# Optimization experiments

Measured on AMD Instinct MI355X. Metric: run time of the kernel, lower is better.

Reference implementation:

```python
import jax, jax.numpy as jnp
import numpy as np
from jax import lax

N = 16384
K = 16
EPS = 1e-5


def setup_inputs() -> dict:
    key = jax.random.key(0)
    ks = jax.random.split(key, 10)

    def w(k, shape):
        fan_in = shape[0]
        return jax.random.normal(k, shape, jnp.float32) / np.sqrt(fan_in)

    return {
        "pos": jax.random.normal(ks[0], (N, 3), jnp.float32),
        "normal": jax.random.normal(ks[1], (N, 3), jnp.float32),
        # conv1 mlp: Linear(9,64) -> GroupNorm(8,64) -> ReLU -> Linear(64,64)
        "W1a": w(ks[2], (9, 64)), "b1a": jnp.zeros((64,), jnp.float32),
        "g1": jnp.ones((64,), jnp.float32), "beta1": jnp.zeros((64,), jnp.float32),
        "W1b": w(ks[3], (64, 64)), "b1b": jnp.zeros((64,), jnp.float32),
        # conv2 mlp: Linear(67,64) -> GroupNorm(8,64) -> ReLU -> Linear(64,64)
        "W2a": w(ks[4], (67, 64)), "b2a": jnp.zeros((64,), jnp.float32),
        "g2": jnp.ones((64,), jnp.float32), "beta2": jnp.zeros((64,), jnp.float32),
        "W2b": w(ks[5], (64, 64)), "b2b": jnp.zeros((64,), jnp.float32),
        # conv3 mlp: Linear(67,128) -> GroupNorm(16,128) -> ReLU -> Linear(128,128)
        "W3a": w(ks[6], (67, 128)), "b3a": jnp.zeros((128,), jnp.float32),
        "g3": jnp.ones((128,), jnp.float32), "beta3": jnp.zeros((128,), jnp.float32),
        "W3b": w(ks[7], (128, 128)), "b3b": jnp.zeros((128,), jnp.float32),
    }


def knn_graph(pos, k):
    # [N,N] squared distances; loop=True -> self is included (distance 0).
    sq = jnp.sum(pos * pos, axis=1)
    d2 = sq[:, None] + sq[None, :] - 2.0 * (pos @ pos.T)
    _, nbr = lax.top_k(-d2, k)  # [N,k] neighbor (source) indices per target node
    return nbr


def group_norm(h, gamma, beta, groups):
    # h: [N,k,C]; normalize each group of channels per edge sample.
    n, k, c = h.shape
    hg = h.reshape(n, k, groups, c // groups)
    mu = hg.mean(axis=-1, keepdims=True)
    var = hg.var(axis=-1, keepdims=True)
    hg = (hg - mu) * lax.rsqrt(var + EPS)
    return hg.reshape(n, k, c) * gamma + beta


def pointnet_conv(x, pos, nbr, Wa, ba, gamma, beta, Wb, bb, groups):
    # message: concat(x_j, pos_j - pos_i), MLP per edge, max-aggregate over neighbors
    xj = x[nbr]                              # [N,k,C_in]
    rel = pos[nbr] - pos[:, None, :]         # [N,k,3]
    m = jnp.concatenate([xj, rel], axis=-1)  # [N,k,C_in+3]
    h = m @ Wa + ba
    h = jax.nn.relu(group_norm(h, gamma, beta, groups))
    h = h @ Wb + bb
    return jnp.max(h, axis=1)                # [N,C_out]


def reference(pos, normal, W1a, b1a, g1, beta1, W1b, b1b,
              W2a, b2a, g2, beta2, W2b, b2b,
              W3a, b3a, g3, beta3, W3b, b3b):
    nbr = knn_graph(pos, K)
    h = jnp.concatenate([pos, normal], axis=-1)  # [N,6]
    h1 = jax.nn.relu(pointnet_conv(h, pos, nbr, W1a, b1a, g1, beta1, W1b, b1b, 8))
    h2 = jax.nn.relu(pointnet_conv(h1, pos, nbr, W2a, b2a, g2, beta2, W2b, b2b, 8))
    h3 = jax.nn.relu(pointnet_conv(h2, pos, nbr, W3a, b3a, g3, beta3, W3b, b3b, 16))
    return (h1, h2, h3)
```

## Files before the change

kernel.cpp:

```cpp
#include <hip/hip_runtime.h>
#include <hip/hip_bf16.h>
#include <stdint.h>

typedef unsigned long long u64;
typedef unsigned int u32;
typedef __attribute__((ext_vector_type(8))) short bf16x8;
typedef __attribute__((ext_vector_type(8))) unsigned short u16x8;
typedef __attribute__((ext_vector_type(4))) float f32x4;

__device__ __forceinline__ float ldv(const void* p, size_t idx, int mode) {
  return mode ? __bfloat162float(((const __hip_bfloat16*)p)[idx])
              : ((const float*)p)[idx];
}
__device__ __forceinline__ void stv(void* p, size_t idx, int mode, float v) {
  if (mode) ((__hip_bfloat16*)p)[idx] = __float2bfloat16(v);
  else      ((float*)p)[idx] = v;
}
__device__ __forceinline__ unsigned short f2bfb(float f) {
  u32 u = __float_as_uint(f);
  u32 r = u + 0x7fffu + ((u >> 16) & 1u);
  return (unsigned short)(r >> 16);
}
__device__ __forceinline__ float bfb2f(unsigned short b) {
  return __uint_as_float((u32)b << 16);
}
__device__ __forceinline__ u64 shfl64(u64 v, int src) {
  int lo = __shfl((int)(u32)(v & 0xffffffffu), src, 64);
  int hi = __shfl((int)(u32)(v >> 32), src, 64);
  return ((u64)(u32)hi << 32) | (u32)lo;
}
__device__ __forceinline__ u64 shflxor64(u64 v, int m) {
  int lo = __shfl_xor((int)(u32)(v & 0xffffffffu), m, 64);
  int hi = __shfl_xor((int)(u32)(v >> 32), m, 64);
  return ((u64)(u32)hi << 32) | (u32)lo;
}
__device__ __forceinline__ u64 shfl64w16(u64 v, int src) {
  int lo = __shfl((int)(u32)(v & 0xffffffffu), src, 16);
  int hi = __shfl((int)(u32)(v >> 32), src, 16);
  return ((u64)(u32)hi << 32) | (u32)lo;
}

__global__ void PointNetSimple_61409442398998_kernel() {}

struct CvtEnt { const void* src; float* dst; int n; };
struct CvtArgs { CvtEnt e[12]; };
struct WEnt { const void* src; unsigned short* dst; int K, N, Kpad; };
struct WArgs { WEnt e[6]; };

__global__ void setup_kernel(const void* __restrict__ pos,
                             const void* __restrict__ nrm,
                             WArgs wa, CvtArgs ca,
                             int* __restrict__ flag,
                             float4* __restrict__ pos4,
                             float* __restrict__ h0, int n) {
  const unsigned short* u16p = (const unsigned short*)pos;
  int cnt = 0;
  for (int k = 0; k < 32; ++k) {
    int e = (u16p[k] >> 7) & 0xff;
    if (e >= 110 && e <= 140) cnt++;
  }
  const int mode = (cnt >= 26) ? 1 : 0;

  const int nprep = n >> 8;
  const int b = blockIdx.x;
  if (b < nprep) {
    int i = b * 256 + threadIdx.x;
    float x = ldv(pos, 3*(size_t)i+0, mode);
    float y = ldv(pos, 3*(size_t)i+1, mode);
    float z = ldv(pos, 3*(size_t)i+2, mode);
    pos4[i] = make_float4(x, y, z, x*x + y*y + z*z);
    h0[6*(size_t)i+0] = x; h0[6*(size_t)i+1] = y; h0[6*(size_t)i+2] = z;
    h0[6*(size_t)i+3] = ldv(nrm, 3*(size_t)i+0, mode);
    h0[6*(size_t)i+4] = ldv(nrm, 3*(size_t)i+1, mode);
    h0[6*(size_t)i+5] = ldv(nrm, 3*(size_t)i+2, mode);
  } else {
    int r = b - nprep;
    if (r < 6) {
      WEnt ent = wa.e[r];
      for (int t = threadIdx.x; t < ent.N * ent.Kpad; t += blockDim.x) {
        int nn = t / ent.Kpad;
        int k  = t - nn * ent.Kpad;
        float v = (k < ent.K) ? ldv(ent.src, (size_t)k * ent.N + nn, mode) : 0.0f;
        ent.dst[t] = f2bfb(v);
      }
      if (r == 0 && threadIdx.x == 0) flag[0] = mode;
    } else {
      for (int t2 = 0; t2 < 12; ++t2) {
        CvtEnt ent = ca.e[t2];
        for (int t = threadIdx.x; t < ent.n; t += blockDim.x)
          ent.dst[t] = ldv(ent.src, t, mode);
      }
    }
  }
}

#define KNN_TPB 512
#define KNN_WPB 8
#define KCH 1024

__device__ __forceinline__ void knn_flush(u64* __restrict__ wbuf, int& cnt,
                                          u64& val, u64& t15, float& th,
                                          int lane) {
  u64 cand = (lane < cnt) ? wbuf[lane] : ~0ull;
#pragma unroll
  for (int k = 2; k <= 64; k <<= 1) {
#pragma unroll
    for (int j = k >> 1; j > 0; j >>= 1) {
      u64 other = shflxor64(cand, j);
      bool up    = ((lane & k) == 0) || (k == 64);
      bool lower = ((lane & j) == 0);
      bool keepMin = (up == lower);
      u64 mn = cand < other ? cand : other;
      u64 mx = cand < other ? other : cand;
      cand = keepMin ? mn : mx;
    }
  }
  u64 rev = shfl64w16(cand, 15 - (lane & 15));
  u64 lo = val < rev ? val : rev;
#pragma unroll
  for (int j = 8; j > 0; j >>= 1) {
    u64 other = shflxor64(lo, j);
    bool lower = ((lane & j) == 0);
    u64 mn = lo < other ? lo : other;
    u64 mx = lo < other ? other : lo;
    lo = lower ? mn : mx;
  }
  val = (lane < 16) ? lo : ~0ull;
  t15 = shfl64(val, 15);
  th = __uint_as_float((u32)(t15 >> 32));
  cnt = 0;
}

__global__ __launch_bounds__(KNN_TPB) void knn4_kernel(
    const float4* __restrict__ pos4, int* __restrict__ nbr, int n) {
  __shared__ float4 sp[2][KCH];
  __shared__ u64 buf[KNN_WPB][72];
  const int tid  = threadIdx.x;
  const int lane = tid & 63;
  const int wid  = tid >> 6;
  const int i    = blockIdx.x * KNN_WPB + wid;
  const float4 pi = pos4[i];
  u64* wbuf = &buf[wid][0];

  u64 val = ~0ull;
  u64 t15 = ~0ull;
  float th = 3.4e38f;
  int cnt = 0;

  for (int t = tid; t < KCH; t += KNN_TPB) sp[0][t] = pos4[t];
  __syncthreads();

  const int nch = n / KCH;
  for (int c = 0; c < nch; ++c) {
    const int cur = c & 1;
    float4 pre0, pre1;
    const bool more = (c + 1 < nch);
    if (more) {
      pre0 = pos4[(size_t)(c+1)*KCH + tid];
      pre1 = pos4[(size_t)(c+1)*KCH + KNN_TPB + tid];
    }
#pragma unroll 2
    for (int t = 0; t < KCH; t += 64) {
      float4 a = sp[cur][t + lane];
      float d2 = (pi.w + a.w) - 2.0f*(pi.x*a.x + pi.y*a.y + pi.z*a.z);
      d2 = fmaxf(d2, 0.0f);
      bool pass = (d2 <= th);
      u64 bal = __ballot(pass);
      if (bal) {
        int pc = __popcll(bal);
        if (cnt + pc > 64) knn_flush(wbuf, cnt, val, t15, th, lane);
        u32 mb = __builtin_amdgcn_mbcnt_lo((u32)bal, 0u);
        mb = __builtin_amdgcn_mbcnt_hi((u32)(bal >> 32), mb);
        if (pass)
          wbuf[cnt + mb] = ((u64)__float_as_uint(d2) << 32) | (u32)(c*KCH + t + lane);
        cnt += pc;
      }
    }
    if (more) {
      sp[cur^1][tid] = pre0;
      sp[cur^1][KNN_TPB + tid] = pre1;
    }
    __syncthreads();
  }
  knn_flush(wbuf, cnt, val, t15, th, lane);
  if (lane < 16) nbr[(size_t)i*16 + lane] = (int)(val & 0xffffffffu);
}

template<int CIN, int CMID, int KT1, int NT, int KT2>
__global__ __launch_bounds__(256, 4) void conv_mfma3_kernel(
    const float* __restrict__ xin,
    const float4* __restrict__ pos4,
    const int* __restrict__ nbr,
    const int* __restrict__ flag,
    const unsigned short* __restrict__ WaT,
    const unsigned short* __restrict__ WbT,
    const float* __restrict__ baf,
    const float* __restrict__ gmf,
    const float* __restrict__ btf,
    const float* __restrict__ bbf,
    float* __restrict__ xout,
    void* __restrict__ bout, size_t out_off)
{
  constexpr int K1PAD = KT1 * 32;
  constexpr int SB = CMID + 8;

  __shared__ unsigned short msgB[128 * SB];
  __shared__ __align__(16) unsigned short stageb[4][32][24];

  const int tid  = threadIdx.x;
  const int lane = tid & 63;
  const int w    = tid >> 6;
  const int quad = lane >> 4;
  const int cl   = lane & 15;
  const int node0 = blockIdx.x * 8;
  const int mode = flag[0];

  bf16x8 afr[2][KT1];
#pragma unroll
  for (int mt = 0; mt < 2; ++mt) {
    const int node = node0 + w*2 + mt;
    const int j = nbr[(size_t)node*16 + cl];
    const float4 pin = pos4[node];
    const float4 pj = pos4[j];
    const float rx = pj.x - pin.x, ry = pj.y - pin.y, rz = pj.z - pin.z;
    if constexpr (CIN == 64) {
#pragma unroll
      for (int kt = 0; kt < 2; ++kt) {
        const float* p = &xin[(size_t)j*64 + kt*32 + quad*8];
        float4 a = *(const float4*)p;
        float4 b = *(const float4*)(p + 4);
        unsigned short o[8] = {f2bfb(a.x), f2bfb(a.y), f2bfb(a.z), f2bfb(a.w),
                               f2bfb(b.x), f2bfb(b.y), f2bfb(b.z), f2bfb(b.w)};
        afr[mt][kt] = *(bf16x8*)o;
      }
      unsigned short o[8] = {0,0,0,0,0,0,0,0};
      if (quad == 0) { o[0] = f2bfb(rx); o[1] = f2bfb(ry); o[2] = f2bfb(rz); }
      afr[mt][KT1-1] = *(bf16x8*)o;
    } else {
      unsigned short o[8] = {0,0,0,0,0,0,0,0};
      if (quad == 0) {
        const float* p = &xin[(size_t)j*6];
        o[0] = f2bfb(p[0]); o[1] = f2bfb(p[1]); o[2] = f2bfb(p[2]);
        o[3] = f2bfb(p[3]); o[4] = f2bfb(p[4]); o[5] = f2bfb(p[5]);
        o[6] = f2bfb(rx);   o[7] = f2bfb(ry);
      } else if (quad == 1) {
        o[0] = f2bfb(rz);
      }
      afr[mt][0] = *(bf16x8*)o;
    }
  }

  f32x4 acc1[2][NT];
#pragma unroll
  for (int mt = 0; mt < 2; ++mt)
#pragma unroll
    for (int nt = 0; nt < NT; ++nt) acc1[mt][nt] = (f32x4){0.f, 0.f, 0.f, 0.f};
#pragma unroll
  for (int kt = 0; kt < KT1; ++kt)
#pragma unroll
    for (int nt = 0; nt < NT; ++nt) {
      bf16x8 bfr = *(const bf16x8*)&WaT[(size_t)(nt*16 + cl) * K1PAD + kt*32 + quad*8];
      acc1[0][nt] = __builtin_amdgcn_mfma_f32_16x16x32_bf16(afr[0][kt], bfr, acc1[0][nt], 0, 0, 0);
      acc1[1][nt] = __builtin_amdgcn_mfma_f32_16x16x32_bf16(afr[1][kt], bfr, acc1[1][nt], 0, 0, 0);
    }

#pragma unroll
  for (int nt = 0; nt < NT; ++nt) {
    float bac = baf[nt*16 + cl];
#pragma unroll
    for (int mt = 0; mt < 2; ++mt)
#pragma unroll
      for (int reg = 0; reg < 4; ++reg)
        stageb[w][mt*16 + quad*4 + reg][cl] = f2bfb(acc1[mt][nt][reg] + bac);
    asm volatile("" ::: "memory");
    {
      int row = lane >> 1, gl = lane & 1;
      u16x8 hv = *(const u16x8*)&stageb[w][row][gl*8];
      float vv[8];
#pragma unroll
      for (int e = 0; e < 8; ++e) vv[e] = bfb2f(hv[e]);
      float s = 0.f, q = 0.f;
#pragma unroll
      for (int e = 0; e < 8; ++e) { s += vv[e]; q += vv[e]*vv[e]; }
      float mu = s * 0.125f;
      float var = q * 0.125f - mu * mu;
      float inv = rsqrtf(fmaxf(var, 0.0f) + 1e-5f);
      int cb = nt*16 + gl*8;
      unsigned short o[8];
#pragma unroll
      for (int e = 0; e < 8; ++e) {
        float t = (vv[e] - mu) * inv * gmf[cb+e] + btf[cb+e];
        o[e] = f2bfb(fmaxf(t, 0.0f));
      }
      *(bf16x8*)&msgB[(w*32 + row) * SB + cb] = *(bf16x8*)o;
    }
    asm volatile("" ::: "memory");
  }

  f32x4 acc2[2][NT];
#pragma unroll
  for (int mt = 0; mt < 2; ++mt)
#pragma unroll
    for (int nt = 0; nt < NT; ++nt) acc2[mt][nt] = (f32x4){0.f, 0.f, 0.f, 0.f};
#pragma unroll
  for (int kt = 0; kt < KT2; ++kt) {
    bf16x8 af0 = *(const bf16x8*)&msgB[(w*32 + cl)      * SB + kt*32 + quad*8];
    bf16x8 af1 = *(const bf16x8*)&msgB[(w*32 + 16 + cl) * SB + kt*32 + quad*8];
#pragma unroll
    for (int nt = 0; nt < NT; ++nt) {
      bf16x8 bfr = *(const bf16x8*)&WbT[(size_t)(nt*16 + cl) * CMID + kt*32 + quad*8];
      acc2[0][nt] = __builtin_amdgcn_mfma_f32_16x16x32_bf16(af0, bfr, acc2[0][nt], 0, 0, 0);
      acc2[1][nt] = __builtin_amdgcn_mfma_f32_16x16x32_bf16(af1, bfr, acc2[1][nt], 0, 0, 0);
    }
  }

#pragma unroll
  for (int mt = 0; mt < 2; ++mt) {
    int node = node0 + w*2 + mt;
#pragma unroll
    for (int nt = 0; nt < NT; ++nt) {
      float m = fmaxf(fmaxf(acc2[mt][nt][0], acc2[mt][nt][1]),
                      fmaxf(acc2[mt][nt][2], acc2[mt][nt][3]));
      m = fmaxf(m, __shfl_xor(m, 16, 64));
      m = fmaxf(m, __shfl_xor(m, 32, 64));
      float v = fmaxf(m + bbf[nt*16 + cl], 0.0f);
      if (quad == 0) {
        size_t oi = (size_t)node * CMID + nt*16 + cl;
        if (xout) xout[oi] = v;
        stv(bout, out_off + oi, mode, v);
      }
    }
  }
}

extern "C" void kernel_launch(void* const* d_in, const int* in_sizes, int n_in,
                              void* d_out, int out_size, void* d_ws, size_t ws_size,
                              hipStream_t stream) {
  (void)n_in; (void)ws_size; (void)in_sizes;
  int n = out_size / 256;
  if (n <= 0 || (n & 255)) n = 16384;

  float* ws = (float*)d_ws;
  int*    flag = (int*)ws;
  float4* pos4 = (float4*)(ws + 16);
  float*  h0   = ws + 16 + (size_t)4*n;
  float*  h1   = ws + 16 + (size_t)10*n;
  float*  h2   = ws + 16 + (size_t)74*n;
  int*    nbr  = (int*)(ws + 16 + (size_t)138*n);
  float*  vbuf = ws + 16 + (size_t)154*n;
  unsigned short* wtbuf = (unsigned short*)(vbuf + 1024);

  const int vsz[12] = {64,64,64,64, 64,64,64,64, 128,128,128,128};
  const int vsrc[12] = {3,4,5,7, 9,10,11,13, 15,16,17,19};
  CvtArgs ca;
  float* vptr[12];
  {
    int off = 0;
    for (int t = 0; t < 12; ++t) {
      ca.e[t].src = d_in[vsrc[t]];
      ca.e[t].dst = vbuf + off;
      ca.e[t].n   = vsz[t];
      vptr[t] = vbuf + off;
      off += vsz[t];
    }
  }
  const int wK[6]    = {9, 64, 67, 64, 67, 128};
  const int wN[6]    = {64, 64, 64, 64, 128, 128};
  const int wKp[6]   = {32, 64, 96, 64, 96, 128};
  const int wsrc[6]  = {2, 6, 8, 12, 14, 18};
  WArgs wa;
  unsigned short* wptr[6];
  {
    int off = 0;
    for (int t = 0; t < 6; ++t) {
      wa.e[t].src  = d_in[wsrc[t]];
      wa.e[t].dst  = wtbuf + off;
      wa.e[t].K    = wK[t];
      wa.e[t].N    = wN[t];
      wa.e[t].Kpad = wKp[t];
      wptr[t] = wtbuf + off;
      off += wN[t] * wKp[t];
    }
  }

  setup_kernel<<<n/256 + 7, 256, 0, stream>>>(
      d_in[0], d_in[1], wa, ca, flag, pos4, h0, n);
  knn4_kernel<<<n/KNN_WPB, KNN_TPB, 0, stream>>>(pos4, nbr, n);

  conv_mfma3_kernel<6, 64, 1, 4, 2><<<n/8, 256, 0, stream>>>(
      h0, pos4, nbr, flag, wptr[0], wptr[1],
      vptr[0], vptr[1], vptr[2], vptr[3], h1, d_out, (size_t)0);
  conv_mfma3_kernel<64, 64, 3, 4, 2><<<n/8, 256, 0, stream>>>(
      h1, pos4, nbr, flag, wptr[2], wptr[3],
      vptr[4], vptr[5], vptr[6], vptr[7], h2, d_out, (size_t)n*64);
  conv_mfma3_kernel<64, 128, 3, 8, 4><<<n/8, 256, 0, stream>>>(
      h2, pos4, nbr, flag, wptr[4], wptr[5],
      vptr[8], vptr[9], vptr[10], vptr[11], (float*)nullptr, d_out, (size_t)n*128);
}
```

Baseline: 373.8 us.

## Replace brute-force kNN with uniform-grid cell search and store intermediates as bf16

```diff
diff --git a/kernel.cpp b/kernel.cpp
--- a/kernel.cpp
+++ b/kernel.cpp
@@ -42,17 +42,38 @@
 
 __global__ void PointNetSimple_61409442398998_kernel() {}
 
+#define GRD 64
+#define GRD3 (GRD*GRD*GRD)
+#define GLO (-4.75f)
+#define GH 0.1484375f
+#define GINVH 6.7368421053f
+
+__device__ __forceinline__ int cell_of(float x, float y, float z,
+                                       int& gx, int& gy, int& gz) {
+  gx = min(GRD-1, max(0, (int)floorf((x - GLO) * GINVH)));
+  gy = min(GRD-1, max(0, (int)floorf((y - GLO) * GINVH)));
+  gz = min(GRD-1, max(0, (int)floorf((z - GLO) * GINVH)));
+  return (gz*GRD + gy)*GRD + gx;
+}
+
 struct CvtEnt { const void* src; float* dst; int n; };
 struct CvtArgs { CvtEnt e[12]; };
 struct WEnt { const void* src; unsigned short* dst; int K, N, Kpad; };
 struct WArgs { WEnt e[6]; };
+
+__global__ void zero_kernel(u32* __restrict__ p) {
+  int i = blockIdx.x * blockDim.x + threadIdx.x;
+  ((uint4*)p)[i] = make_uint4(0u, 0u, 0u, 0u);
+}
 
 __global__ void setup_kernel(const void* __restrict__ pos,
                              const void* __restrict__ nrm,
                              WArgs wa, CvtArgs ca,
                              int* __restrict__ flag,
                              float4* __restrict__ pos4,
-                             float* __restrict__ h0, int n) {
+                             float* __restrict__ h0,
+                             u32* __restrict__ cellId,
+                             u32* __restrict__ cellCnt, int n) {
   const unsigned short* u16p = (const unsigned short*)pos;
   int cnt = 0;
   for (int k = 0; k < 32; ++k) {
@@ -73,6 +94,10 @@
     h0[6*(size_t)i+3] = ldv(nrm, 3*(size_t)i+0, mode);
     h0[6*(size_t)i+4] = ldv(nrm, 3*(size_t)i+1, mode);
     h0[6*(size_t)i+5] = ldv(nrm, 3*(size_t)i+2, mode);
+    int gx, gy, gz;
+    int cid = cell_of(x, y, z, gx, gy, gz);
+    cellId[i] = (u32)cid;
+    atomicAdd(&cellCnt[cid], 1u);
   } else {
     int r = b - nprep;
     if (r < 6) {
@@ -94,9 +119,57 @@
   }
 }
 
-#define KNN_TPB 512
+__global__ __launch_bounds__(256) void scanA_kernel(const u32* __restrict__ cnt,
+                                                    u32* __restrict__ off,
+                                                    u32* __restrict__ blkSum) {
+  __shared__ u32 s[256];
+  const int b = blockIdx.x, t = threadIdx.x;
+  const int base = b*1024 + t*4;
+  u32 c0 = cnt[base], c1 = cnt[base+1], c2 = cnt[base+2], c3 = cnt[base+3];
+  u32 sum = c0+c1+c2+c3;
+  s[t] = sum;
+  __syncthreads();
+  u32 v = sum;
+  for (int d = 1; d < 256; d <<= 1) {
+    u32 o = (t >= d) ? s[t-d] : 0u;
+    __syncthreads();
+    v += o; s[t] = v;
+    __syncthreads();
+  }
+  u32 excl = v - sum;
+  off[base]   = excl;
+  off[base+1] = excl + c0;
+  off[base+2] = excl + c0 + c1;
+  off[base+3] = excl + c0 + c1 + c2;
+  if (t == 255) blkSum[b] = v;
+}
+
+__global__ void scanB_kernel(u32* __restrict__ blkSum) {
+  __shared__ u32 s[256];
+  const int t = threadIdx.x;
+  u32 x = blkSum[t]; s[t] = x; __syncthreads();
+  u32 v = x;
+  for (int d = 1; d < 256; d <<= 1) {
+    u32 o = (t >= d) ? s[t-d] : 0u;
+    __syncthreads();
+    v += o; s[t] = v;
+    __syncthreads();
+  }
+  blkSum[t] = v - x;
+}
+
+__global__ void scatter_kernel(const u32* __restrict__ cellId,
+                               u32* __restrict__ cellOff,
+                               const u32* __restrict__ blkScan,
+                               u32* __restrict__ ptIdx, int n) {
+  int i = blockIdx.x * blockDim.x + threadIdx.x;
+  if (i >= n) return;
+  u32 c = cellId[i];
+  u32 slot = atomicAdd(&cellOff[c], 1u);
+  ptIdx[blkScan[c >> 10] + slot] = (u32)i;
+}
+
 #define KNN_WPB 8
-#define KCH 1024
 
 __device__ __forceinline__ void knn_flush(u64* __restrict__ wbuf, int& cnt,
                                           u64& val, u64& t15, float& th,
@@ -127,68 +200,88 @@
   }
   val = (lane < 16) ? lo : ~0ull;
   t15 = shfl64(val, 15);
-  th = __uint_as_float((u32)(t15 >> 32));
+  if (t15 != ~0ull) th = __uint_as_float((u32)(t15 >> 32));
   cnt = 0;
 }
 
-__global__ __launch_bounds__(KNN_TPB) void knn4_kernel(
-    const float4* __restrict__ pos4, int* __restrict__ nbr, int n) {
-  __shared__ float4 sp[2][KCH];
+__global__ __launch_bounds__(512) void knng_kernel(
+    const float4* __restrict__ pos4,
+    const u32* __restrict__ cellCnt,
+    const u32* __restrict__ cellOff,
+    const u32* __restrict__ blkScan,
+    const u32* __restrict__ ptIdx,
+    int* __restrict__ nbr, int n) {
   __shared__ u64 buf[KNN_WPB][72];
-  const int tid  = threadIdx.x;
-  const int lane = tid & 63;
-  const int wid  = tid >> 6;
-  const int i    = blockIdx.x * KNN_WPB + wid;
+  const int tid = threadIdx.x, lane = tid & 63, wid = tid >> 6;
+  const int i = blockIdx.x * KNN_WPB + wid;
   const float4 pi = pos4[i];
   u64* wbuf = &buf[wid][0];
 
-  u64 val = ~0ull;
-  u64 t15 = ~0ull;
+  u64 val = ~0ull, t15 = ~0ull;
   float th = 3.4e38f;
   int cnt = 0;
 
-  for (int t = tid; t < KCH; t += KNN_TPB) sp[0][t] = pos4[t];
-  __syncthreads();
-
-  const int nch = n / KCH;
-  for (int c = 0; c < nch; ++c) {
-    const int cur = c & 1;
-    float4 pre0, pre1;
-    const bool more = (c + 1 < nch);
-    if (more) {
-      pre0 = pos4[(size_t)(c+1)*KCH + tid];
-      pre1 = pos4[(size_t)(c+1)*KCH + KNN_TPB + tid];
-    }
-#pragma unroll 2
-    for (int t = 0; t < KCH; t += 64) {
-      float4 a = sp[cur][t + lane];
-      float d2 = (pi.w + a.w) - 2.0f*(pi.x*a.x + pi.y*a.y + pi.z*a.z);
-      d2 = fmaxf(d2, 0.0f);
-      bool pass = (d2 <= th);
-      u64 bal = __ballot(pass);
-      if (bal) {
-        int pc = __popcll(bal);
-        if (cnt + pc > 64) knn_flush(wbuf, cnt, val, t15, th, lane);
-        u32 mb = __builtin_amdgcn_mbcnt_lo((u32)bal, 0u);
-        mb = __builtin_amdgcn_mbcnt_hi((u32)(bal >> 32), mb);
-        if (pass)
-          wbuf[cnt + mb] = ((u64)__float_as_uint(d2) << 32) | (u32)(c*KCH + t + lane);
-        cnt += pc;
-      }
-    }
-    if (more) {
-      sp[cur^1][tid] = pre0;
-      sp[cur^1][KNN_TPB + tid] = pre1;
-    }
-    __syncthreads();
-  }
-  knn_flush(wbuf, cnt, val, t15, th, lane);
+  int gx, gy, gz;
+  cell_of(pi.x, pi.y, pi.z, gx, gy, gz);
+
+  for (int r = 0; r < GRD; ++r) {
+    if (r >= 1 && t15 != ~0ull) {
+      float bound = (float)(r - 1) * GH;
+      if (bound * bound > th + 1e-4f) break;
+    }
+    const int S = 2*r + 1;
+    const int S2 = S*S;
+    const int S3 = S2*S;
+    for (int l0 = 0; l0 < S3; l0 += 64) {
+      int l = l0 + lane;
+      int myCnt = 0; u32 myStart = 0;
+      if (l < S3) {
+        int dz = l / S2;
+        int rem = l - dz*S2;
+        int dy = rem / S;
+        int dx = rem - dy*S;
+        dx -= r; dy -= r; dz -= r;
+        int cheb = max(abs(dx), max(abs(dy), abs(dz)));
+        int cx = gx + dx, cy = gy + dy, cz = gz + dz;
+        if (cheb == r && cx >= 0 && cx < GRD && cy >= 0 && cy < GRD &&
+            cz >= 0 && cz < GRD) {
+          int c = (cz*GRD + cy)*GRD + cx;
+          myCnt = (int)cellCnt[c];
+          myStart = blkScan[c >> 10] + cellOff[c] - (u32)myCnt;
+        }
+      }
+      for (int k = 0; ; ++k) {
+        bool has = (k < myCnt);
+        if (__ballot(has) == 0ull) break;
+        float d2 = 3.4e38f; u32 j = 0xffffffffu;
+        if (has) {
+          j = ptIdx[myStart + k];
+          float4 a = pos4[j];
+          float dd = (pi.w + a.w) - 2.0f*(pi.x*a.x + pi.y*a.y + pi.z*a.z);
+          d2 = fmaxf(dd, 0.0f);
+        }
+        bool pass = has && (d2 <= th);
+        u64 bal = __ballot(pass);
+        if (bal) {
+          int pc = __popcll(bal);
+          if (cnt + pc > 64) knn_flush(wbuf, cnt, val, t15, th, lane);
+          u32 mb = __builtin_amdgcn_mbcnt_lo((u32)bal, 0u);
+          mb = __builtin_amdgcn_mbcnt_hi((u32)(bal >> 32), mb);
+          if (pass)
+            wbuf[cnt + mb] = ((u64)__float_as_uint(d2) << 32) | j;
+          cnt += pc;
+        }
+      }
+    }
+    knn_flush(wbuf, cnt, val, t15, th, lane);
+  }
   if (lane < 16) nbr[(size_t)i*16 + lane] = (int)(val & 0xffffffffu);
 }
 
 template<int CIN, int CMID, int KT1, int NT, int KT2>
-__global__ __launch_bounds__(256, 4) void conv_mfma3_kernel(
-    const float* __restrict__ xin,
+__global__ __launch_bounds__(256, 4) void conv_mfma4_kernel(
+    const float* __restrict__ xf,
+    const unsigned short* __restrict__ xb,
     const float4* __restrict__ pos4,
     const int* __restrict__ nbr,
     const int* __restrict__ flag,
@@ -198,7 +291,7 @@
     const float* __restrict__ gmf,
     const float* __restrict__ btf,
     const float* __restrict__ bbf,
-    float* __restrict__ xout,
+    unsigned short* __restrict__ xoutb,
     void* __restrict__ bout, size_t out_off)
 {
   constexpr int K1PAD = KT1 * 32;
@@ -225,21 +318,15 @@
     const float rx = pj.x - pin.x, ry = pj.y - pin.y, rz = pj.z - pin.z;
     if constexpr (CIN == 64) {
 #pragma unroll
-      for (int kt = 0; kt < 2; ++kt) {
-        const float* p = &xin[(size_t)j*64 + kt*32 + quad*8];
-        float4 a = *(const float4*)p;
-        float4 b = *(const float4*)(p + 4);
-        unsigned short o[8] = {f2bfb(a.x), f2bfb(a.y), f2bfb(a.z), f2bfb(a.w),
-                               f2bfb(b.x), f2bfb(b.y), f2bfb(b.z), f2bfb(b.w)};
-        afr[mt][kt] = *(bf16x8*)o;
-      }
+      for (int kt = 0; kt < 2; ++kt)
+        afr[mt][kt] = *(const bf16x8*)&xb[(size_t)j*64 + kt*32 + quad*8];
       unsigned short o[8] = {0,0,0,0,0,0,0,0};
       if (quad == 0) { o[0] = f2bfb(rx); o[1] = f2bfb(ry); o[2] = f2bfb(rz); }
       afr[mt][KT1-1] = *(bf16x8*)o;
     } else {
       unsigned short o[8] = {0,0,0,0,0,0,0,0};
       if (quad == 0) {
-        const float* p = &xin[(size_t)j*6];
+        const float* p = &xf[(size_t)j*6];
         o[0] = f2bfb(p[0]); o[1] = f2bfb(p[1]); o[2] = f2bfb(p[2]);
         o[3] = f2bfb(p[3]); o[4] = f2bfb(p[4]); o[5] = f2bfb(p[5]);
         o[6] = f2bfb(rx);   o[7] = f2bfb(ry);
@@ -326,7 +413,7 @@
       float v = fmaxf(m + bbf[nt*16 + cl], 0.0f);
       if (quad == 0) {
         size_t oi = (size_t)node * CMID + nt*16 + cl;
-        if (xout) xout[oi] = v;
+        if (xoutb) xoutb[oi] = f2bfb(v);
         stv(bout, out_off + oi, mode, v);
       }
     }
@@ -341,14 +428,19 @@
   if (n <= 0 || (n & 255)) n = 16384;
 
   float* ws = (float*)d_ws;
-  int*    flag = (int*)ws;
-  float4* pos4 = (float4*)(ws + 16);
-  float*  h0   = ws + 16 + (size_t)4*n;
-  float*  h1   = ws + 16 + (size_t)10*n;
-  float*  h2   = ws + 16 + (size_t)74*n;
-  int*    nbr  = (int*)(ws + 16 + (size_t)138*n);
-  float*  vbuf = ws + 16 + (size_t)154*n;
+  int*    flag    = (int*)ws;
+  float4* pos4    = (float4*)(ws + 16);
+  float*  h0      = ws + 16 + (size_t)4*n;
+  int*    nbr     = (int*)(ws + 16 + (size_t)10*n);
+  unsigned short* h1b = (unsigned short*)(ws + 16 + (size_t)26*n);
+  unsigned short* h2b = (unsigned short*)(ws + 16 + (size_t)58*n);
+  float*  vbuf    = ws + 16 + (size_t)90*n;
   unsigned short* wtbuf = (unsigned short*)(vbuf + 1024);
+  u32*    cellCnt = (u32*)(ws + 16 + (size_t)90*n + 23552);
+  u32*    cellOff = cellCnt + GRD3;
+  u32*    blkScan = cellOff + GRD3;
+  u32*    cellId  = blkScan + 512;
+  u32*    ptIdx   = cellId + n;
 
   const int vsz[12] = {64,64,64,64, 64,64,64,64, 128,128,128,128};
   const int vsrc[12] = {3,4,5,7, 9,10,11,13, 15,16,17,19};
@@ -383,17 +475,23 @@
     }
   }
 
+  zero_kernel<<<GRD3/4/256, 256, 0, stream>>>(cellCnt);
   setup_kernel<<<n/256 + 7, 256, 0, stream>>>(
-      d_in[0], d_in[1], wa, ca, flag, pos4, h0, n);
-  knn4_kernel<<<n/KNN_WPB, KNN_TPB, 0, stream>>>(pos4, nbr, n);
-
-  conv_mfma3_kernel<6, 64, 1, 4, 2><<<n/8, 256, 0, stream>>>(
-      h0, pos4, nbr, flag, wptr[0], wptr[1],
-      vptr[0], vptr[1], vptr[2], vptr[3], h1, d_out, (size_t)0);
-  conv_mfma3_kernel<64, 64, 3, 4, 2><<<n/8, 256, 0, stream>>>(
-      h1, pos4, nbr, flag, wptr[2], wptr[3],
-      vptr[4], vptr[5], vptr[6], vptr[7], h2, d_out, (size_t)n*64);
-  conv_mfma3_kernel<64, 128, 3, 8, 4><<<n/8, 256, 0, stream>>>(
-      h2, pos4, nbr, flag, wptr[4], wptr[5],
-      vptr[8], vptr[9], vptr[10], vptr[11], (float*)nullptr, d_out, (size_t)n*128);
-}
+      d_in[0], d_in[1], wa, ca, flag, pos4, h0, cellId, cellCnt, n);
+  scanA_kernel<<<256, 256, 0, stream>>>(cellCnt, cellOff, blkScan);
+  scanB_kernel<<<1, 256, 0, stream>>>(blkScan);
+  scatter_kernel<<<n/256, 256, 0, stream>>>(cellId, cellOff, blkScan, ptIdx, n);
+  knng_kernel<<<n/KNN_WPB, 512, 0, stream>>>(
+      pos4, cellCnt, cellOff, blkScan, ptIdx, nbr, n);
+
+  conv_mfma4_kernel<6, 64, 1, 4, 2><<<n/8, 256, 0, stream>>>(
+      h0, (const unsigned short*)nullptr, pos4, nbr, flag, wptr[0], wptr[1],
+      vptr[0], vptr[1], vptr[2], vptr[3], h1b, d_out, (size_t)0);
+  conv_mfma4_kernel<64, 64, 3, 4, 2><<<n/8, 256, 0, stream>>>(
+      (const float*)nullptr, h1b, pos4, nbr, flag, wptr[2], wptr[3],
+      vptr[4], vptr[5], vptr[6], vptr[7], h2b, d_out, (size_t)n*64);
+  conv_mfma4_kernel<64, 128, 3, 8, 4><<<n/8, 256, 0, stream>>>(
+      (const float*)nullptr, h2b, pos4, nbr, flag, wptr[4], wptr[5],
+      vptr[8], vptr[9], vptr[10], vptr[11],
+      (unsigned short*)nullptr, d_out, (size_t)n*128);
+}
```

After: 805.9 us. +115.6%, slower.

## Store intermediate features as bf16 and stage GroupNorm directly in msgB

Applied to the files above, without the earlier changes.

```diff
diff --git a/kernel.cpp b/kernel.cpp
--- a/kernel.cpp
+++ b/kernel.cpp
@@ -187,8 +187,9 @@
 }
 
 template<int CIN, int CMID, int KT1, int NT, int KT2>
-__global__ __launch_bounds__(256, 4) void conv_mfma3_kernel(
-    const float* __restrict__ xin,
+__global__ __launch_bounds__(256, 4) void conv_mfma5_kernel(
+    const float* __restrict__ xf,
+    const unsigned short* __restrict__ xb,
     const float4* __restrict__ pos4,
     const int* __restrict__ nbr,
     const int* __restrict__ flag,
@@ -198,14 +199,13 @@
     const float* __restrict__ gmf,
     const float* __restrict__ btf,
     const float* __restrict__ bbf,
-    float* __restrict__ xout,
+    unsigned short* __restrict__ xoutb,
     void* __restrict__ bout, size_t out_off)
 {
   constexpr int K1PAD = KT1 * 32;
   constexpr int SB = CMID + 8;
 
   __shared__ unsigned short msgB[128 * SB];
-  __shared__ __align__(16) unsigned short stageb[4][32][24];
 
   const int tid  = threadIdx.x;
   const int lane = tid & 63;
@@ -225,21 +225,15 @@
     const float rx = pj.x - pin.x, ry = pj.y - pin.y, rz = pj.z - pin.z;
     if constexpr (CIN == 64) {
 #pragma unroll
-      for (int kt = 0; kt < 2; ++kt) {
-        const float* p = &xin[(size_t)j*64 + kt*32 + quad*8];
-        float4 a = *(const float4*)p;
-        float4 b = *(const float4*)(p + 4);
-        unsigned short o[8] = {f2bfb(a.x), f2bfb(a.y), f2bfb(a.z), f2bfb(a.w),
-                               f2bfb(b.x), f2bfb(b.y), f2bfb(b.z), f2bfb(b.w)};
-        afr[mt][kt] = *(bf16x8*)o;
-      }
+      for (int kt = 0; kt < 2; ++kt)
+        afr[mt][kt] = *(const bf16x8*)&xb[(size_t)j*64 + kt*32 + quad*8];
       unsigned short o[8] = {0,0,0,0,0,0,0,0};
       if (quad == 0) { o[0] = f2bfb(rx); o[1] = f2bfb(ry); o[2] = f2bfb(rz); }
       afr[mt][KT1-1] = *(bf16x8*)o;
     } else {
       unsigned short o[8] = {0,0,0,0,0,0,0,0};
       if (quad == 0) {
-        const float* p = &xin[(size_t)j*6];
+        const float* p = &xf[(size_t)j*6];
         o[0] = f2bfb(p[0]); o[1] = f2bfb(p[1]); o[2] = f2bfb(p[2]);
         o[3] = f2bfb(p[3]); o[4] = f2bfb(p[4]); o[5] = f2bfb(p[5]);
         o[6] = f2bfb(rx);   o[7] = f2bfb(ry);
@@ -271,11 +265,18 @@
     for (int mt = 0; mt < 2; ++mt)
 #pragma unroll
       for (int reg = 0; reg < 4; ++reg)
-        stageb[w][mt*16 + quad*4 + reg][cl] = f2bfb(acc1[mt][nt][reg] + bac);
-    asm volatile("" ::: "memory");
-    {
-      int row = lane >> 1, gl = lane & 1;
-      u16x8 hv = *(const u16x8*)&stageb[w][row][gl*8];
+        msgB[(w*32 + mt*16 + quad*4 + reg) * SB + nt*16 + cl] =
+            f2bfb(acc1[mt][nt][reg] + bac);
+  }
+  asm volatile("" ::: "memory");
+
+  {
+    const int row = lane >> 1, gl = lane & 1;
+#pragma unroll
+    for (int nt = 0; nt < NT; ++nt) {
+      const int cb = nt*16 + gl*8;
+      unsigned short* p = &msgB[(w*32 + row) * SB + cb];
+      u16x8 hv = *(const u16x8*)p;
       float vv[8];
 #pragma unroll
       for (int e = 0; e < 8; ++e) vv[e] = bfb2f(hv[e]);
@@ -285,17 +286,16 @@
       float mu = s * 0.125f;
       float var = q * 0.125f - mu * mu;
       float inv = rsqrtf(fmaxf(var, 0.0f) + 1e-5f);
-      int cb = nt*16 + gl*8;
       unsigned short o[8];
 #pragma unroll
       for (int e = 0; e < 8; ++e) {
         float t = (vv[e] - mu) * inv * gmf[cb+e] + btf[cb+e];
         o[e] = f2bfb(fmaxf(t, 0.0f));
       }
-      *(bf16x8*)&msgB[(w*32 + row) * SB + cb] = *(bf16x8*)o;
-    }
-    asm volatile("" ::: "memory");
-  }
+      *(bf16x8*)p = *(bf16x8*)o;
+    }
+  }
+  asm volatile("" ::: "memory");
 
   f32x4 acc2[2][NT];
 #pragma unroll
@@ -326,7 +326,7 @@
       float v = fmaxf(m + bbf[nt*16 + cl], 0.0f);
       if (quad == 0) {
         size_t oi = (size_t)node * CMID + nt*16 + cl;
-        if (xout) xout[oi] = v;
+        if (xoutb) xoutb[oi] = f2bfb(v);
         stv(bout, out_off + oi, mode, v);
       }
     }
@@ -341,13 +341,13 @@
   if (n <= 0 || (n & 255)) n = 16384;
 
   float* ws = (float*)d_ws;
-  int*    flag = (int*)ws;
-  float4* pos4 = (float4*)(ws + 16);
-  float*  h0   = ws + 16 + (size_t)4*n;
-  float*  h1   = ws + 16 + (size_t)10*n;
-  float*  h2   = ws + 16 + (size_t)74*n;
-  int*    nbr  = (int*)(ws + 16 + (size_t)138*n);
-  float*  vbuf = ws + 16 + (size_t)154*n;
+  int*    flag    = (int*)ws;
+  float4* pos4    = (float4*)(ws + 16);
+  float*  h0      = ws + 16 + (size_t)4*n;
+  int*    nbr     = (int*)(ws + 16 + (size_t)10*n);
+  unsigned short* h1b = (unsigned short*)(ws + 16 + (size_t)26*n);
+  unsigned short* h2b = (unsigned short*)(ws + 16 + (size_t)58*n);
+  float*  vbuf    = ws + 16 + (size_t)90*n;
   unsigned short* wtbuf = (unsigned short*)(vbuf + 1024);
 
   const int vsz[12] = {64,64,64,64, 64,64,64,64, 128,128,128,128};
@@ -387,13 +387,14 @@
       d_in[0], d_in[1], wa, ca, flag, pos4, h0, n);
   knn4_kernel<<<n/KNN_WPB, KNN_TPB, 0, stream>>>(pos4, nbr, n);
 
-  conv_mfma3_kernel<6, 64, 1, 4, 2><<<n/8, 256, 0, stream>>>(
-      h0, pos4, nbr, flag, wptr[0], wptr[1],
-      vptr[0], vptr[1], vptr[2], vptr[3], h1, d_out, (size_t)0);
-  conv_mfma3_kernel<64, 64, 3, 4, 2><<<n/8, 256, 0, stream>>>(
-      h1, pos4, nbr, flag, wptr[2], wptr[3],
-      vptr[4], vptr[5], vptr[6], vptr[7], h2, d_out, (size_t)n*64);
-  conv_mfma3_kernel<64, 128, 3, 8, 4><<<n/8, 256, 0, stream>>>(
-      h2, pos4, nbr, flag, wptr[4], wptr[5],
-      vptr[8], vptr[9], vptr[10], vptr[11], (float*)nullptr, d_out, (size_t)n*128);
-}
+  conv_mfma5_kernel<6, 64, 1, 4, 2><<<n/8, 256, 0, stream>>>(
+      h0, (const unsigned short*)nullptr, pos4, nbr, flag, wptr[0], wptr[1],
+      vptr[0], vptr[1], vptr[2], vptr[3], h1b, d_out, (size_t)0);
+  conv_mfma5_kernel<64, 64, 3, 4, 2><<<n/8, 256, 0, stream>>>(
+      (const float*)nullptr, h1b, pos4, nbr, flag, wptr[2], wptr[3],
+      vptr[4], vptr[5], vptr[6], vptr[7], h2b, d_out, (size_t)n*64);
+  conv_mfma5_kernel<64, 128, 3, 8, 4><<<n/8, 256, 0, stream>>>(
+      (const float*)nullptr, h2b, pos4, nbr, flag, wptr[4], wptr[5],
+      vptr[8], vptr[9], vptr[10], vptr[11],
+      (unsigned short*)nullptr, d_out, (size_t)n*128);
+}
```

After: 371.7 us. No clear change (-0.6%).
